# Performance work log

Measured on AMD Instinct MI355X. Metric: run time of the kernel, lower is better.

## Reference

```python
import jax, jax.numpy as jnp
import numpy as np

B, S, E, HEADS, LATENT = 8, 4096, 2048, 16, 64
HEAD_SIZE = E // HEADS  # 128
NEG = -1e20


def setup_inputs() -> dict:
    key = jax.random.key(0)
    k0, k1, k2, k3, k4 = jax.random.split(key, 5)
    return {
        "x": jax.random.normal(k0, (B, S, E), dtype=jnp.float32) * 0.02,
        "W_dkv": jax.random.normal(k1, (LATENT, E), dtype=jnp.float32) * 0.02,
        "W_k": jax.random.normal(k2, (HEAD_SIZE, LATENT), dtype=jnp.float32) * 0.02,
        "W_v": jax.random.normal(k3, (HEAD_SIZE, LATENT), dtype=jnp.float32) * 0.02,
        "W_q": jax.random.normal(k4, (HEAD_SIZE, E), dtype=jnp.float32) * 0.02,
    }


def reference(x, W_dkv, W_k, W_v, W_q):
    # x: [B,S,E]; nn.Linear computes x @ W.T (weight layout [out,in])
    head_size = W_k.shape[0]
    latent = jnp.einsum("bse,le->bsl", x, W_dkv)        # latent KV cache [B,S,L]
    absorbed_q = W_q.T @ W_k                              # [E,H] @ [H,L] -> [E,L]
    q_res = jnp.einsum("bse,el->bsl", x, absorbed_q)     # [B,S,L]
    scale = head_size ** -0.5
    scores = jnp.einsum("bql,bkl->bqk", q_res, latent) * scale  # [B,S,S]
    seq = x.shape[1]
    causal = jnp.tril(jnp.ones((seq, seq), dtype=bool))
    scores = jnp.where(causal, scores, NEG)
    attn = jax.nn.softmax(scores, axis=-1)               # dropout skipped (eval mode)
    v = jnp.einsum("bsl,hl->bsh", latent, W_v)           # compressed V [B,S,H]
    out = jnp.einsum("bqk,bkh->bqh", attn, v)            # [B,S,head_size]
    return out, latent  # latent == kv_cache returned by the module
```

## Files before the change

### kernel.cpp

```cpp
#include <hip/hip_runtime.h>
#include <hip/hip_bf16.h>

#define NB 8
#define NS 4096
#define NE 2048
#define NL 64
#define NH 128
#define NM (NB*NS)
#define NQT (NS/64)

typedef unsigned short ushort_t;
typedef __attribute__((ext_vector_type(4))) float f32x4;
typedef __attribute__((ext_vector_type(8))) __bf16 bf16x8;
typedef __attribute__((ext_vector_type(8))) unsigned short u16x8;
typedef __attribute__((ext_vector_type(4))) unsigned short u16x4;

#define SCALE2 0.1275174537f

__device__ __forceinline__ float fast_exp2(float x) {
    return __builtin_amdgcn_exp2f(x);
}

__device__ __forceinline__ unsigned short f2bf(float f) {
    union { float f; unsigned u; } v; v.f = f;
    unsigned u = v.u + 0x7fffu + ((v.u >> 16) & 1u);
    return (unsigned short)(u >> 16);
}

__device__ __forceinline__ int swz(int row, int colbyte) {
    return (row * 128 + colbyte) ^ ((row & 7) << 4);
}

__device__ __forceinline__ void wg_barrier() {
    asm volatile("s_waitcnt lgkmcnt(0)" ::: "memory");
    __builtin_amdgcn_s_barrier();
    __builtin_amdgcn_sched_barrier(0);
}

__global__ __launch_bounds__(256) void prep_kernel(
    const float* __restrict__ Wdkv, const float* __restrict__ Wk,
    const float* __restrict__ Wq, ushort_t* __restrict__ WcatT)
{
    __shared__ float wk[128 * 64];
    const int t = threadIdx.x;
    for (int i = t; i < 128 * 64; i += 256) wk[i] = Wk[i];
    __syncthreads();
    const int e = blockIdx.x * 256 + t;
    const int l0 = blockIdx.y * 16;
    float acc[16];
    #pragma unroll
    for (int l = 0; l < 16; ++l) acc[l] = 0.f;
    for (int h = 0; h < 128; ++h) {
        float q = Wq[h * NE + e];
        #pragma unroll
        for (int l = 0; l < 16; ++l) acc[l] += q * wk[h * 64 + l0 + l];
    }
    for (int l = 0; l < 16; ++l) WcatT[(64 + l0 + l) * NE + e] = f2bf(acc[l] * SCALE2);
    for (int l = 0; l < 16; ++l) WcatT[(l0 + l) * NE + e] = f2bf(Wdkv[(l0 + l) * NE + e]);
}

__global__ __launch_bounds__(256) void proj_kernel(
    const float* __restrict__ x, const ushort_t* __restrict__ WcatT,
    const float* __restrict__ Wv,
    float* __restrict__ latent_out, ushort_t* __restrict__ k_bf,
    ushort_t* __restrict__ q_bf, ushort_t* __restrict__ v_t)
{
    __shared__ ushort_t As[2][64 * 64];
    __shared__ ushort_t Bs[2][128 * 64];
    const int tid = threadIdx.x;
    const int w = tid >> 6, lane = tid & 63, lg = lane >> 4, li = lane & 15;
    const int m0 = blockIdx.x * 64;
    const int wm = (w >> 1) * 32, wn = (w & 1) * 64;
    const int srow = tid >> 3, scol = tid & 7;

    f32x4 acc[2][4];
    #pragma unroll
    for (int i = 0; i < 2; ++i)
        #pragma unroll
        for (int j = 0; j < 4; ++j) acc[i][j] = f32x4{0.f, 0.f, 0.f, 0.f};

    f32x4 a0reg[2][2], a1reg[2][2];
    u16x8 b0reg[4], b1reg[4];

#define PLOAD(k0, AR, BR) do { \
    _Pragma("unroll") for (int p = 0; p < 2; ++p) { \
        const float* gp = x + (long)(m0 + srow + 32 * p) * NE + (k0) + scol * 8; \
        AR[p][0] = *reinterpret_cast<const f32x4*>(gp); \
        AR[p][1] = *reinterpret_cast<const f32x4*>(gp + 4); } \
    _Pragma("unroll") for (int p = 0; p < 4; ++p) \
        BR[p] = *reinterpret_cast<const u16x8*>(WcatT + (long)(srow + 32 * p) * NE + (k0) + scol * 8); \
} while (0)

#define PWRITE(AR, BR, buf) do { \
    _Pragma("unroll") for (int p = 0; p < 2; ++p) { \
        u16x8 h; \
        _Pragma("unroll") for (int j = 0; j < 4; ++j) { h[j] = f2bf(AR[p][0][j]); h[4 + j] = f2bf(AR[p][1][j]); } \
        *reinterpret_cast<u16x8*>(reinterpret_cast<char*>(As[buf]) + swz(srow + 32 * p, scol * 16)) = h; } \
    _Pragma("unroll") for (int p = 0; p < 4; ++p) \
        *reinterpret_cast<u16x8*>(reinterpret_cast<char*>(Bs[buf]) + swz(srow + 32 * p, scol * 16)) = BR[p]; \
} while (0)

    auto compute = [&](int buf) {
        #pragma unroll
        for (int c = 0; c < 2; ++c) {
            bf16x8 af[2], bfv[4];
            #pragma unroll
            for (int mf = 0; mf < 2; ++mf)
                af[mf] = *reinterpret_cast<const bf16x8*>(
                    reinterpret_cast<const char*>(As[buf]) + swz(wm + 16 * mf + li, c * 64 + lg * 16));
            #pragma unroll
            for (int nf = 0; nf < 4; ++nf)
                bfv[nf] = *reinterpret_cast<const bf16x8*>(
                    reinterpret_cast<const char*>(Bs[buf]) + swz(wn + 16 * nf + li, c * 64 + lg * 16));
            #pragma unroll
            for (int mf = 0; mf < 2; ++mf)
                #pragma unroll
                for (int nf = 0; nf < 4; ++nf)
                    acc[mf][nf] = __builtin_amdgcn_mfma_f32_16x16x32_bf16(
                        af[mf], bfv[nf], acc[mf][nf], 0, 0, 0);
        }
    };

    PLOAD(0, a0reg, b0reg);
    PLOAD(64, a1reg, b1reg);
    PWRITE(a0reg, b0reg, 0);
    wg_barrier();

    for (int ks = 0; ks < 32; ks += 2) {
        if (ks + 2 < 32) PLOAD((ks + 2) * 64, a0reg, b0reg);
        compute(0);
        PWRITE(a1reg, b1reg, 1);
        wg_barrier();
        if (ks + 3 < 32) PLOAD((ks + 3) * 64, a1reg, b1reg);
        compute(1);
        if (ks + 2 < 32) PWRITE(a0reg, b0reg, 0);
        wg_barrier();
    }

    const int b = m0 >> 12, s0 = m0 & 4095;
    #pragma unroll
    for (int mf = 0; mf < 2; ++mf) {
        #pragma unroll
        for (int nf = 0; nf < 4; ++nf) {
            int col = wn + 16 * nf + li;
            #pragma unroll
            for (int r = 0; r < 4; ++r) {
                int row = m0 + wm + 16 * mf + 4 * lg + r;
                float v = acc[mf][nf][r];
                if (wn == 0) {
                    latent_out[(long)row * NL + col] = v;
                    k_bf[(long)row * NL + col] = f2bf(v);
                    *reinterpret_cast<ushort_t*>(reinterpret_cast<char*>(As[0]) +
                        swz(wm + 16 * mf + 4 * lg + r, col * 2)) = f2bf(v);
                } else {
                    q_bf[(long)row * NL + (col - 64)] = f2bf(v);
                }
            }
        }
    }
    {
        const int r = tid >> 1, hf = tid & 1;
        const float* wp = Wv + r * 64 + hf * 32;
        #pragma unroll
        for (int q = 0; q < 2; ++q) {
            f32x4 w0 = *reinterpret_cast<const f32x4*>(wp + q * 16);
            f32x4 w1 = *reinterpret_cast<const f32x4*>(wp + q * 16 + 4);
            f32x4 w2 = *reinterpret_cast<const f32x4*>(wp + q * 16 + 8);
            f32x4 w3 = *reinterpret_cast<const f32x4*>(wp + q * 16 + 12);
            u16x8 h0, h1;
            #pragma unroll
            for (int j = 0; j < 4; ++j) {
                h0[j] = f2bf(w0[j]); h0[4 + j] = f2bf(w1[j]);
                h1[j] = f2bf(w2[j]); h1[4 + j] = f2bf(w3[j]);
            }
            *reinterpret_cast<u16x8*>(reinterpret_cast<char*>(Bs[0]) + swz(r, hf * 64 + q * 32)) = h0;
            *reinterpret_cast<u16x8*>(reinterpret_cast<char*>(Bs[0]) + swz(r, hf * 64 + q * 32 + 16)) = h1;
        }
    }
    wg_barrier();
    f32x4 vacc[2][4];
    #pragma unroll
    for (int i = 0; i < 2; ++i)
        #pragma unroll
        for (int j = 0; j < 4; ++j) vacc[i][j] = f32x4{0.f, 0.f, 0.f, 0.f};
    #pragma unroll
    for (int c = 0; c < 2; ++c) {
        bf16x8 af[2], bfv[4];
        #pragma unroll
        for (int mf = 0; mf < 2; ++mf)
            af[mf] = *reinterpret_cast<const bf16x8*>(
                reinterpret_cast<const char*>(Bs[0]) + swz(32 * w + 16 * mf + li, c * 64 + lg * 16));
        #pragma unroll
        for (int nf = 0; nf < 4; ++nf)
            bfv[nf] = *reinterpret_cast<const bf16x8*>(
                reinterpret_cast<const char*>(As[0]) + swz(16 * nf + li, c * 64 + lg * 16));
        #pragma unroll
        for (int mf = 0; mf < 2; ++mf)
            #pragma unroll
            for (int nf = 0; nf < 4; ++nf)
                vacc[mf][nf] = __builtin_amdgcn_mfma_f32_16x16x32_bf16(
                    af[mf], bfv[nf], vacc[mf][nf], 0, 0, 0);
    }
    #pragma unroll
    for (int mf = 0; mf < 2; ++mf)
        #pragma unroll
        for (int nf = 0; nf < 4; ++nf)
            #pragma unroll
            for (int r = 0; r < 4; ++r)
                v_t[(long)(b * 128 + 32 * w + 16 * mf + 4 * lg + r) * NS + s0 + 16 * nf + li] =
                    f2bf(vacc[mf][nf][r]);
}

__global__ __launch_bounds__(256) void attn_kernel(
    const ushort_t* __restrict__ q_bf, const ushort_t* __restrict__ k_bf,
    const ushort_t* __restrict__ v_t, float* __restrict__ Opart,
    float* __restrict__ lpart, float* __restrict__ mpart)
{
    __shared__ ushort_t Ks[2][64 * 64];
    __shared__ ushort_t Vts[2][128 * 64];
    const int tid = threadIdx.x;
    const int w = tid >> 6, lane = tid & 63, lg = lane >> 4, li = lane & 15;
    const int l = blockIdx.x;
    const int b = l & 7;
    const int j = l >> 3;
    const int h = j >> 6;
    const int p_ = j & 63;
    const int k_ = p_ >> 1, e_ = p_ & 1, kk = (k_ & 15) * 2;
    const int qt = (k_ >> 4) ? (e_ ? kk + 1 : 63 - kk) : (e_ ? 62 - kk : kk);
    const int niter = (qt + 2 - h) >> 1;
    const bool hasdiag = ((qt - h) & 1) == 0;
    const int Q0 = qt << 6;
    const int srow = tid >> 3, scol = tid & 7;
    const int vc0 = 64 * ((scol >> 1) & 1) + 32 * (scol & 1) + 8 * (scol >> 2);

    const long qrow = (long)b * NS + Q0 + 16 * w + li;
    bf16x8 qf[2];
    qf[0] = *reinterpret_cast<const bf16x8*>(q_bf + qrow * NL + 0 + lg * 8);
    qf[1] = *reinterpret_cast<const bf16x8*>(q_bf + qrow * NL + 32 + lg * 8);

    float m_r = -3.0e38f, l_r = 0.f;
    f32x4 oacc[8];
    #pragma unroll
    for (int n = 0; n < 8; ++n) oacc[n] = f32x4{0.f, 0.f, 0.f, 0.f};

    u16x8 k0reg[2], v0reg[4], k1reg[2], v1reg[4];

#define ALOAD(kv0, KR, VR) do { \
    _Pragma("unroll") for (int p = 0; p < 2; ++p) \
        KR[p] = *reinterpret_cast<const u16x8*>(k_bf + ((long)b * NS + (kv0) + srow + 32 * p) * NL + scol * 8); \
    _Pragma("unroll") for (int p = 0; p < 4; ++p) \
        VR[p] = *reinterpret_cast<const u16x8*>(v_t + (long)(b * 128 + srow + 32 * p) * NS + (kv0) + scol * 8); \
} while (0)

#define AWRITE(KR, VR, buf) do { \
    _Pragma("unroll") for (int p = 0; p < 2; ++p) \
        *reinterpret_cast<u16x8*>(reinterpret_cast<char*>(Ks[buf]) + swz(srow + 32 * p, scol * 16)) = KR[p]; \
    _Pragma("unroll") for (int p = 0; p < 4; ++p) { \
        u16x4 lo = {VR[p][0], VR[p][1], VR[p][2], VR[p][3]}; \
        u16x4 hi = {VR[p][4], VR[p][5], VR[p][6], VR[p][7]}; \
        *reinterpret_cast<u16x4*>(reinterpret_cast<char*>(Vts[buf]) + swz(srow + 32 * p, vc0)) = lo; \
        *reinterpret_cast<u16x4*>(reinterpret_cast<char*>(Vts[buf]) + swz(srow + 32 * p, vc0 + 16)) = hi; \
    } \
} while (0)

    auto compute = [&](int buf, bool diag) {
        const char* Kb = reinterpret_cast<const char*>(Ks[buf]);
        const char* Vb = reinterpret_cast<const char*>(Vts[buf]);
        f32x4 s[4];
        #pragma unroll
        for (int f = 0; f < 4; ++f) s[f] = f32x4{0.f, 0.f, 0.f, 0.f};
        __builtin_amdgcn_s_setprio(1);
        #pragma unroll
        for (int c = 0; c < 2; ++c)
            #pragma unroll
            for (int f = 0; f < 4; ++f) {
                bf16x8 a = *reinterpret_cast<const bf16x8*>(Kb + swz(16 * f + li, c * 64 + lg * 16));
                s[f] = __builtin_amdgcn_mfma_f32_16x16x32_bf16(a, qf[c], s[f], 0, 0, 0);
            }
        __builtin_amdgcn_s_setprio(0);
        float p[16];
        float mx = -3.0e38f;
        #pragma unroll
        for (int f = 0; f < 4; ++f)
            #pragma unroll
            for (int r = 0; r < 4; ++r) {
                float v = s[f][r];
                if (diag && (16 * f + 4 * lg + r) > (16 * w + li)) v = -3.0e38f;
                p[f * 4 + r] = v;
                mx = fmaxf(mx, v);
            }
        if (!__all(mx <= m_r + 8.f)) {
            float mxf = fmaxf(mx, __shfl_xor(mx, 16));
            mxf = fmaxf(mxf, __shfl_xor(mxf, 32));
            float m_new = fmaxf(m_r, mxf);
            float corr = fast_exp2(m_r - m_new);
            m_r = m_new;
            l_r *= corr;
            float corrO[4];
            #pragma unroll
            for (int r = 0; r < 4; ++r)
                corrO[r] = __shfl(corr, (lane & 48) | (4 * lg + r));
            #pragma unroll
            for (int n = 0; n < 8; ++n)
                #pragma unroll
                for (int r = 0; r < 4; ++r) oacc[n][r] *= corrO[r];
        }
        float rs = 0.f;
        #pragma unroll
        for (int i = 0; i < 16; ++i) { p[i] = fast_exp2(p[i] - m_r); rs += p[i]; }
        l_r += rs;
        unsigned pw[8];
        #pragma unroll
        for (int f = 0; f < 4; ++f)
            #pragma unroll
            for (int hh = 0; hh < 2; ++hh)
                asm("v_cvt_pk_bf16_f32 %0, %1, %2"
                    : "=v"(pw[2 * f + hh]) : "v"(p[4 * f + 2 * hh]), "v"(p[4 * f + 2 * hh + 1]));
        union { unsigned u[4]; bf16x8 v; } pa0, pa1;
        pa0.u[0] = pw[0]; pa0.u[1] = pw[1]; pa0.u[2] = pw[4]; pa0.u[3] = pw[5];
        pa1.u[0] = pw[2]; pa1.u[1] = pw[3]; pa1.u[2] = pw[6]; pa1.u[3] = pw[7];
        __builtin_amdgcn_s_setprio(1);
        #pragma unroll
        for (int c = 0; c < 2; ++c) {
            bf16x8 pa = c ? pa1.v : pa0.v;
            #pragma unroll
            for (int n = 0; n < 8; ++n) {
                bf16x8 vb = *reinterpret_cast<const bf16x8*>(Vb + swz(16 * n + li, c * 64 + lg * 16));
                oacc[n] = __builtin_amdgcn_mfma_f32_16x16x32_bf16(pa, vb, oacc[n], 0, 0, 0);
            }
        }
        __builtin_amdgcn_s_setprio(0);
    };

    if (niter > 0) {
        ALOAD(h * 64, k0reg, v0reg);
        if (niter >= 2) ALOAD((h + 2) * 64, k1reg, v1reg);
        AWRITE(k0reg, v0reg, 0);
        wg_barrier();
        for (int i = 0; i < niter; i += 2) {
            if (i + 2 < niter) ALOAD((h + 2 * (i + 2)) * 64, k0reg, v0reg);
            compute(0, hasdiag && (i == niter - 1));
            if (i + 1 < niter) AWRITE(k1reg, v1reg, 1);
            wg_barrier();
            if (i + 1 >= niter) break;
            if (i + 3 < niter) ALOAD((h + 2 * (i + 3)) * 64, k1reg, v1reg);
            compute(1, hasdiag && (i + 1 == niter - 1));
            if (i + 2 < niter) AWRITE(k0reg, v0reg, 0);
            wg_barrier();
        }
    }

    l_r += __shfl_xor(l_r, 16);
    l_r += __shfl_xor(l_r, 32);
    const int IB = ((h * NB + b) << 6) + qt;
    if (lane < 16)  {
        lpart[IB * 64 + 16 * w + li] = l_r;
        mpart[IB * 64 + 16 * w + li] = m_r;
    }
    #pragma unroll
    for (int n = 0; n < 8; ++n)
        #pragma unroll
        for (int r = 0; r < 4; ++r)
            Opart[((long)IB * 64 + 16 * w + 4 * lg + r) * NH + 16 * n + li] = oacc[n][r];
}

__global__ __launch_bounds__(256) void merge_kernel(
    const float* __restrict__ Opart, const float* __restrict__ lpart,
    const float* __restrict__ mpart, float* __restrict__ out)
{
    const int blk = blockIdx.x;
    const int b = blk >> 6, qt = blk & 63;
    const int t = threadIdx.x;
    const int row = t >> 2, c0 = (t & 3) * 4;
    const int IB1 = (b << 6) + qt;
    const int IB2 = ((NB + b) << 6) + qt;
    const long r1 = (long)IB1 * 64 + row, r2 = (long)IB2 * 64 + row;
    float l1 = lpart[r1], m1 = mpart[r1];
    float l2 = lpart[r2], m2 = mpart[r2];
    float M = fmaxf(m1, m2);
    float w1 = fast_exp2(m1 - M), w2 = fast_exp2(m2 - M);
    float inv = 1.f / (w1 * l1 + w2 * l2);
    float a1 = w1 * inv, a2 = w2 * inv;
    const float* o1 = Opart + r1 * NH;
    const float* o2 = Opart + r2 * NH;
    float* op = out + ((long)b * NS + qt * 64 + row) * NH;
    #pragma unroll
    for (int jj = 0; jj < 8; ++jj) {
        int col = c0 + 16 * jj;
        f32x4 A = *reinterpret_cast<const f32x4*>(o1 + col);
        f32x4 Bv = *reinterpret_cast<const f32x4*>(o2 + col);
        f32x4 R;
        #pragma unroll
        for (int q = 0; q < 4; ++q) R[q] = A[q] * a1 + Bv[q] * a2;
        *reinterpret_cast<f32x4*>(op + col) = R;
    }
}

extern "C" void kernel_launch(void* const* d_in, const int* in_sizes, int n_in,
                              void* d_out, int out_size, void* d_ws, size_t ws_size,
                              hipStream_t stream) {
    const float* x    = (const float*)d_in[0];
    const float* Wdkv = (const float*)d_in[1];
    const float* Wk   = (const float*)d_in[2];
    const float* Wv   = (const float*)d_in[3];
    const float* Wq   = (const float*)d_in[4];

    float* out = (float*)d_out;
    float* latent_out = out + (long)NM * NH;

    ushort_t* WcatT = (ushort_t*)d_ws;
    ushort_t* q_bf  = WcatT + 128 * NE;
    ushort_t* k_bf  = q_bf + (long)NM * NL;
    ushort_t* v_t   = k_bf + (long)NM * NL;
    float* Opart = (float*)(v_t + (long)NM * NH);
    float* lpart = Opart + (long)2 * NB * NQT * 64 * NH;
    float* mpart = lpart + 2 * NB * NQT * 64;

    hipLaunchKernelGGL(prep_kernel, dim3(NE / 256, 4), dim3(256), 0, stream, Wdkv, Wk, Wq, WcatT);
    hipLaunchKernelGGL(proj_kernel, dim3(NM / 64), dim3(256), 0, stream,
                       x, WcatT, Wv, latent_out, k_bf, q_bf, v_t);
    hipLaunchKernelGGL(attn_kernel, dim3(1024), dim3(256), 0, stream,
                       q_bf, k_bf, v_t, Opart, lpart, mpart);
    hipLaunchKernelGGL(merge_kernel, dim3(NB * NQT), dim3(256), 0, stream,
                       Opart, lpart, mpart, out);
}
```

Measured before the change: 161.1 us.

## Attend over latent values and apply W_v after the softmax merge

Uses associativity (attn @ (latent @ Wv^T) = (attn @ latent) @ Wv^T): the attention kernel now accumulates P·latent in the 64-wide latent space instead of the 128-wide V space. The projection kernel writes a transposed latent (made with an identity-matrix MFMA) rather than computing V, and the merge kernel applies W_v once per query tile with MFMAs. This halves the V tile loads, LDS traffic, PV MFMAs and the partial-output size. In exchange the merge kernel does more work, including an extra bf16 rounding of the merged output before the W_v product.

```diff
diff --git a/kernel.cpp b/kernel.cpp
--- a/kernel.cpp
+++ b/kernel.cpp
@@ -61,9 +61,8 @@
 
 __global__ __launch_bounds__(256) void proj_kernel(
     const float* __restrict__ x, const ushort_t* __restrict__ WcatT,
-    const float* __restrict__ Wv,
     float* __restrict__ latent_out, ushort_t* __restrict__ k_bf,
-    ushort_t* __restrict__ q_bf, ushort_t* __restrict__ v_t)
+    ushort_t* __restrict__ q_bf, ushort_t* __restrict__ kt)
 {
     __shared__ ushort_t As[2][64 * 64];
     __shared__ ushort_t Bs[2][128 * 64];
@@ -158,66 +157,36 @@
             }
         }
     }
-    {
-        const int r = tid >> 1, hf = tid & 1;
-        const float* wp = Wv + r * 64 + hf * 32;
-        #pragma unroll
-        for (int q = 0; q < 2; ++q) {
-            f32x4 w0 = *reinterpret_cast<const f32x4*>(wp + q * 16);
-            f32x4 w1 = *reinterpret_cast<const f32x4*>(wp + q * 16 + 4);
-            f32x4 w2 = *reinterpret_cast<const f32x4*>(wp + q * 16 + 8);
-            f32x4 w3 = *reinterpret_cast<const f32x4*>(wp + q * 16 + 12);
-            u16x8 h0, h1;
-            #pragma unroll
-            for (int j = 0; j < 4; ++j) {
-                h0[j] = f2bf(w0[j]); h0[4 + j] = f2bf(w1[j]);
-                h1[j] = f2bf(w2[j]); h1[4 + j] = f2bf(w3[j]);
-            }
-            *reinterpret_cast<u16x8*>(reinterpret_cast<char*>(Bs[0]) + swz(r, hf * 64 + q * 32)) = h0;
-            *reinterpret_cast<u16x8*>(reinterpret_cast<char*>(Bs[0]) + swz(r, hf * 64 + q * 32 + 16)) = h1;
-        }
-    }
     wg_barrier();
-    f32x4 vacc[2][4];
-    #pragma unroll
-    for (int i = 0; i < 2; ++i)
-        #pragma unroll
-        for (int j = 0; j < 4; ++j) vacc[i][j] = f32x4{0.f, 0.f, 0.f, 0.f};
-    #pragma unroll
-    for (int c = 0; c < 2; ++c) {
-        bf16x8 af[2], bfv[4];
-        #pragma unroll
-        for (int mf = 0; mf < 2; ++mf)
-            af[mf] = *reinterpret_cast<const bf16x8*>(
-                reinterpret_cast<const char*>(Bs[0]) + swz(32 * w + 16 * mf + li, c * 64 + lg * 16));
-        #pragma unroll
-        for (int nf = 0; nf < 4; ++nf)
-            bfv[nf] = *reinterpret_cast<const bf16x8*>(
-                reinterpret_cast<const char*>(As[0]) + swz(16 * nf + li, c * 64 + lg * 16));
-        #pragma unroll
-        for (int mf = 0; mf < 2; ++mf)
-            #pragma unroll
-            for (int nf = 0; nf < 4; ++nf)
-                vacc[mf][nf] = __builtin_amdgcn_mfma_f32_16x16x32_bf16(
-                    af[mf], bfv[nf], vacc[mf][nf], 0, 0, 0);
-    }
-    #pragma unroll
-    for (int mf = 0; mf < 2; ++mf)
-        #pragma unroll
-        for (int nf = 0; nf < 4; ++nf)
-            #pragma unroll
-            for (int r = 0; r < 4; ++r)
-                v_t[(long)(b * 128 + 32 * w + 16 * mf + 4 * lg + r) * NS + s0 + 16 * nf + li] =
-                    f2bf(vacc[mf][nf][r]);
+    union { u16x8 u; bf16x8 v; } iu;
+    #pragma unroll
+    for (int j = 0; j < 8; ++j)
+        iu.u[j] = (lg == (li >> 3) + 2 * (w & 1) && (li & 7) == j)
+                      ? (ushort_t)0x3F80 : (ushort_t)0;
+    const int ckt = w >> 1;
+    f32x4 ktacc[4];
+    #pragma unroll
+    for (int nf = 0; nf < 4; ++nf) {
+        bf16x8 bfv = *reinterpret_cast<const bf16x8*>(
+            reinterpret_cast<const char*>(As[0]) + swz(16 * nf + li, ckt * 64 + lg * 16));
+        ktacc[nf] = __builtin_amdgcn_mfma_f32_16x16x32_bf16(
+            iu.v, bfv, f32x4{0.f, 0.f, 0.f, 0.f}, 0, 0, 0);
+    }
+    #pragma unroll
+    for (int nf = 0; nf < 4; ++nf)
+        #pragma unroll
+        for (int r = 0; r < 4; ++r)
+            kt[(long)(b * 64 + 16 * w + 4 * lg + r) * NS + s0 + 16 * nf + li] =
+                f2bf(ktacc[nf][r]);
 }
 
 __global__ __launch_bounds__(256) void attn_kernel(
     const ushort_t* __restrict__ q_bf, const ushort_t* __restrict__ k_bf,
-    const ushort_t* __restrict__ v_t, float* __restrict__ Opart,
+    const ushort_t* __restrict__ kt, float* __restrict__ Opart,
     float* __restrict__ lpart, float* __restrict__ mpart)
 {
     __shared__ ushort_t Ks[2][64 * 64];
-    __shared__ ushort_t Vts[2][128 * 64];
+    __shared__ ushort_t KTs[2][64 * 64];
     const int tid = threadIdx.x;
     const int w = tid >> 6, lane = tid & 63, lg = lane >> 4, li = lane & 15;
     const int l = blockIdx.x;
@@ -239,33 +208,33 @@
     qf[1] = *reinterpret_cast<const bf16x8*>(q_bf + qrow * NL + 32 + lg * 8);
 
     float m_r = -3.0e38f, l_r = 0.f;
-    f32x4 oacc[8];
-    #pragma unroll
-    for (int n = 0; n < 8; ++n) oacc[n] = f32x4{0.f, 0.f, 0.f, 0.f};
-
-    u16x8 k0reg[2], v0reg[4], k1reg[2], v1reg[4];
-
-#define ALOAD(kv0, KR, VR) do { \
+    f32x4 oacc[4];
+    #pragma unroll
+    for (int n = 0; n < 4; ++n) oacc[n] = f32x4{0.f, 0.f, 0.f, 0.f};
+
+    u16x8 k0reg[2], t0reg[2], k1reg[2], t1reg[2];
+
+#define ALOAD(kv0, KR, TR) do { \
     _Pragma("unroll") for (int p = 0; p < 2; ++p) \
         KR[p] = *reinterpret_cast<const u16x8*>(k_bf + ((long)b * NS + (kv0) + srow + 32 * p) * NL + scol * 8); \
-    _Pragma("unroll") for (int p = 0; p < 4; ++p) \
-        VR[p] = *reinterpret_cast<const u16x8*>(v_t + (long)(b * 128 + srow + 32 * p) * NS + (kv0) + scol * 8); \
+    _Pragma("unroll") for (int p = 0; p < 2; ++p) \
+        TR[p] = *reinterpret_cast<const u16x8*>(kt + (long)(b * 64 + srow + 32 * p) * NS + (kv0) + scol * 8); \
 } while (0)
 
-#define AWRITE(KR, VR, buf) do { \
+#define AWRITE(KR, TR, buf) do { \
     _Pragma("unroll") for (int p = 0; p < 2; ++p) \
         *reinterpret_cast<u16x8*>(reinterpret_cast<char*>(Ks[buf]) + swz(srow + 32 * p, scol * 16)) = KR[p]; \
-    _Pragma("unroll") for (int p = 0; p < 4; ++p) { \
-        u16x4 lo = {VR[p][0], VR[p][1], VR[p][2], VR[p][3]}; \
-        u16x4 hi = {VR[p][4], VR[p][5], VR[p][6], VR[p][7]}; \
-        *reinterpret_cast<u16x4*>(reinterpret_cast<char*>(Vts[buf]) + swz(srow + 32 * p, vc0)) = lo; \
-        *reinterpret_cast<u16x4*>(reinterpret_cast<char*>(Vts[buf]) + swz(srow + 32 * p, vc0 + 16)) = hi; \
+    _Pragma("unroll") for (int p = 0; p < 2; ++p) { \
+        u16x4 lo = {TR[p][0], TR[p][1], TR[p][2], TR[p][3]}; \
+        u16x4 hi = {TR[p][4], TR[p][5], TR[p][6], TR[p][7]}; \
+        *reinterpret_cast<u16x4*>(reinterpret_cast<char*>(KTs[buf]) + swz(srow + 32 * p, vc0)) = lo; \
+        *reinterpret_cast<u16x4*>(reinterpret_cast<char*>(KTs[buf]) + swz(srow + 32 * p, vc0 + 16)) = hi; \
     } \
 } while (0)
 
     auto compute = [&](int buf, bool diag) {
         const char* Kb = reinterpret_cast<const char*>(Ks[buf]);
-        const char* Vb = reinterpret_cast<const char*>(Vts[buf]);
+        const char* Tb = reinterpret_cast<const char*>(KTs[buf]);
         f32x4 s[4];
         #pragma unroll
         for (int f = 0; f < 4; ++f) s[f] = f32x4{0.f, 0.f, 0.f, 0.f};
@@ -301,7 +270,7 @@
             for (int r = 0; r < 4; ++r)
                 corrO[r] = __shfl(corr, (lane & 48) | (4 * lg + r));
             #pragma unroll
-            for (int n = 0; n < 8; ++n)
+            for (int n = 0; n < 4; ++n)
                 #pragma unroll
                 for (int r = 0; r < 4; ++r) oacc[n][r] *= corrO[r];
         }
@@ -324,8 +293,8 @@
         for (int c = 0; c < 2; ++c) {
             bf16x8 pa = c ? pa1.v : pa0.v;
             #pragma unroll
-            for (int n = 0; n < 8; ++n) {
-                bf16x8 vb = *reinterpret_cast<const bf16x8*>(Vb + swz(16 * n + li, c * 64 + lg * 16));
+            for (int n = 0; n < 4; ++n) {
+                bf16x8 vb = *reinterpret_cast<const bf16x8*>(Tb + swz(16 * n + li, c * 64 + lg * 16));
                 oacc[n] = __builtin_amdgcn_mfma_f32_16x16x32_bf16(pa, vb, oacc[n], 0, 0, 0);
             }
         }
@@ -333,19 +302,19 @@
     };
 
     if (niter > 0) {
-        ALOAD(h * 64, k0reg, v0reg);
-        if (niter >= 2) ALOAD((h + 2) * 64, k1reg, v1reg);
-        AWRITE(k0reg, v0reg, 0);
+        ALOAD(h * 64, k0reg, t0reg);
+        if (niter >= 2) ALOAD((h + 2) * 64, k1reg, t1reg);
+        AWRITE(k0reg, t0reg, 0);
         wg_barrier();
         for (int i = 0; i < niter; i += 2) {
-            if (i + 2 < niter) ALOAD((h + 2 * (i + 2)) * 64, k0reg, v0reg);
+            if (i + 2 < niter) ALOAD((h + 2 * (i + 2)) * 64, k0reg, t0reg);
             compute(0, hasdiag && (i == niter - 1));
-            if (i + 1 < niter) AWRITE(k1reg, v1reg, 1);
+            if (i + 1 < niter) AWRITE(k1reg, t1reg, 1);
             wg_barrier();
             if (i + 1 >= niter) break;
-            if (i + 3 < niter) ALOAD((h + 2 * (i + 3)) * 64, k1reg, v1reg);
+            if (i + 3 < niter) ALOAD((h + 2 * (i + 3)) * 64, k1reg, t1reg);
             compute(1, hasdiag && (i + 1 == niter - 1));
-            if (i + 2 < niter) AWRITE(k0reg, v0reg, 0);
+            if (i + 2 < niter) AWRITE(k0reg, t0reg, 0);
             wg_barrier();
         }
     }
@@ -358,41 +327,106 @@
         mpart[IB * 64 + 16 * w + li] = m_r;
     }
     #pragma unroll
-    for (int n = 0; n < 8; ++n)
+    for (int n = 0; n < 4; ++n)
         #pragma unroll
         for (int r = 0; r < 4; ++r)
-            Opart[((long)IB * 64 + 16 * w + 4 * lg + r) * NH + 16 * n + li] = oacc[n][r];
+            Opart[((long)IB * 64 + 16 * w + 4 * lg + r) * NL + 16 * n + li] = oacc[n][r];
 }
 
 __global__ __launch_bounds__(256) void merge_kernel(
     const float* __restrict__ Opart, const float* __restrict__ lpart,
-    const float* __restrict__ mpart, float* __restrict__ out)
+    const float* __restrict__ mpart, const float* __restrict__ Wv,
+    float* __restrict__ out)
 {
+    __shared__ ushort_t Ms[64 * 64];
+    __shared__ ushort_t Wvs[128 * 64];
+    __shared__ float Os[64 * 132];
     const int blk = blockIdx.x;
     const int b = blk >> 6, qt = blk & 63;
-    const int t = threadIdx.x;
-    const int row = t >> 2, c0 = (t & 3) * 4;
-    const int IB1 = (b << 6) + qt;
-    const int IB2 = ((NB + b) << 6) + qt;
-    const long r1 = (long)IB1 * 64 + row, r2 = (long)IB2 * 64 + row;
-    float l1 = lpart[r1], m1 = mpart[r1];
-    float l2 = lpart[r2], m2 = mpart[r2];
-    float M = fmaxf(m1, m2);
-    float w1 = fast_exp2(m1 - M), w2 = fast_exp2(m2 - M);
-    float inv = 1.f / (w1 * l1 + w2 * l2);
-    float a1 = w1 * inv, a2 = w2 * inv;
-    const float* o1 = Opart + r1 * NH;
-    const float* o2 = Opart + r2 * NH;
-    float* op = out + ((long)b * NS + qt * 64 + row) * NH;
-    #pragma unroll
-    for (int jj = 0; jj < 8; ++jj) {
-        int col = c0 + 16 * jj;
-        f32x4 A = *reinterpret_cast<const f32x4*>(o1 + col);
-        f32x4 Bv = *reinterpret_cast<const f32x4*>(o2 + col);
-        f32x4 R;
-        #pragma unroll
-        for (int q = 0; q < 4; ++q) R[q] = A[q] * a1 + Bv[q] * a2;
-        *reinterpret_cast<f32x4*>(op + col) = R;
+    const int tid = threadIdx.x;
+    const int w = tid >> 6, lane = tid & 63, lg = lane >> 4, li = lane & 15;
+
+    {
+        const int r = tid >> 1, hf = tid & 1;
+        const float* wp = Wv + r * 64 + hf * 32;
+        #pragma unroll
+        for (int q = 0; q < 2; ++q) {
+            f32x4 w0 = *reinterpret_cast<const f32x4*>(wp + q * 16);
+            f32x4 w1 = *reinterpret_cast<const f32x4*>(wp + q * 16 + 4);
+            f32x4 w2 = *reinterpret_cast<const f32x4*>(wp + q * 16 + 8);
+            f32x4 w3 = *reinterpret_cast<const f32x4*>(wp + q * 16 + 12);
+            u16x8 h0, h1;
+            #pragma unroll
+            for (int jj = 0; jj < 4; ++jj) {
+                h0[jj] = f2bf(w0[jj]); h0[4 + jj] = f2bf(w1[jj]);
+                h1[jj] = f2bf(w2[jj]); h1[4 + jj] = f2bf(w3[jj]);
+            }
+            *reinterpret_cast<u16x8*>(reinterpret_cast<char*>(Wvs) + swz(r, hf * 64 + q * 32)) = h0;
+            *reinterpret_cast<u16x8*>(reinterpret_cast<char*>(Wvs) + swz(r, hf * 64 + q * 32 + 16)) = h1;
+        }
+    }
+    {
+        const int r = tid >> 2, c0 = (tid & 3) * 16;
+        const long L1 = ((long)((b << 6) + qt)) * 64 + r;
+        const long L2 = ((long)(((NB + b) << 6) + qt)) * 64 + r;
+        float l1 = lpart[L1], m1 = mpart[L1];
+        float l2 = lpart[L2], m2 = mpart[L2];
+        float M = fmaxf(m1, m2);
+        float w1 = fast_exp2(m1 - M), w2 = fast_exp2(m2 - M);
+        float inv = 1.f / (w1 * l1 + w2 * l2);
+        float a1 = w1 * inv, a2 = w2 * inv;
+        const float* o1 = Opart + L1 * NL;
+        const float* o2 = Opart + L2 * NL;
+        #pragma unroll
+        for (int q = 0; q < 4; ++q) {
+            int col = c0 + q * 4;
+            f32x4 A = *reinterpret_cast<const f32x4*>(o1 + col);
+            f32x4 Bv = *reinterpret_cast<const f32x4*>(o2 + col);
+            u16x4 hh;
+            #pragma unroll
+            for (int k = 0; k < 4; ++k) hh[k] = f2bf(A[k] * a1 + Bv[k] * a2);
+            *reinterpret_cast<u16x4*>(reinterpret_cast<char*>(Ms) + swz(r, col * 2)) = hh;
+        }
+    }
+    __syncthreads();
+    f32x4 vacc[2][4];
+    #pragma unroll
+    for (int i = 0; i < 2; ++i)
+        #pragma unroll
+        for (int jj = 0; jj < 4; ++jj) vacc[i][jj] = f32x4{0.f, 0.f, 0.f, 0.f};
+    #pragma unroll
+    for (int c = 0; c < 2; ++c) {
+        bf16x8 af[2], bfv[4];
+        #pragma unroll
+        for (int mf = 0; mf < 2; ++mf)
+            af[mf] = *reinterpret_cast<const bf16x8*>(
+                reinterpret_cast<const char*>(Wvs) + swz(32 * w + 16 * mf + li, c * 64 + lg * 16));
+        #pragma unroll
+        for (int nf = 0; nf < 4; ++nf)
+            bfv[nf] = *reinterpret_cast<const bf16x8*>(
+                reinterpret_cast<const char*>(Ms) + swz(16 * nf + li, c * 64 + lg * 16));
+        #pragma unroll
+        for (int mf = 0; mf < 2; ++mf)
+            #pragma unroll
+            for (int nf = 0; nf < 4; ++nf)
+                vacc[mf][nf] = __builtin_amdgcn_mfma_f32_16x16x32_bf16(
+                    af[mf], bfv[nf], vacc[mf][nf], 0, 0, 0);
+    }
+    #pragma unroll
+    for (int mf = 0; mf < 2; ++mf)
+        #pragma unroll
+        for (int nf = 0; nf < 4; ++nf)
+            #pragma unroll
+            for (int r = 0; r < 4; ++r)
+                Os[(16 * nf + li) * 132 + 32 * w + 16 * mf + 4 * lg + r] = vacc[mf][nf][r];
+    __syncthreads();
+    {
+        const int r = tid >> 2, cb = (tid & 3) * 32;
+        float* op = out + ((long)b * NS + qt * 64 + r) * NH + cb;
+        const float* sp = Os + r * 132 + cb;
+        #pragma unroll
+        for (int q = 0; q < 8; ++q)
+            *reinterpret_cast<f32x4*>(op + 4 * q) = *reinterpret_cast<const f32x4*>(sp + 4 * q);
     }
 }
 
@@ -411,16 +445,16 @@
     ushort_t* WcatT = (ushort_t*)d_ws;
     ushort_t* q_bf  = WcatT + 128 * NE;
     ushort_t* k_bf  = q_bf + (long)NM * NL;
-    ushort_t* v_t   = k_bf + (long)NM * NL;
-    float* Opart = (float*)(v_t + (long)NM * NH);
-    float* lpart = Opart + (long)2 * NB * NQT * 64 * NH;
+    ushort_t* kt    = k_bf + (long)NM * NL;
+    float* Opart = (float*)(kt + (long)NM * NL);
+    float* lpart = Opart + (long)2 * NB * NQT * 64 * NL;
     float* mpart = lpart + 2 * NB * NQT * 64;
 
     hipLaunchKernelGGL(prep_kernel, dim3(NE / 256, 4), dim3(256), 0, stream, Wdkv, Wk, Wq, WcatT);
     hipLaunchKernelGGL(proj_kernel, dim3(NM / 64), dim3(256), 0, stream,
-                       x, WcatT, Wv, latent_out, k_bf, q_bf, v_t);
+                       x, WcatT, latent_out, k_bf, q_bf, kt);
     hipLaunchKernelGGL(attn_kernel, dim3(1024), dim3(256), 0, stream,
-                       q_bf, k_bf, v_t, Opart, lpart, mpart);
+                       q_bf, k_bf, kt, Opart, lpart, mpart);
     hipLaunchKernelGGL(merge_kernel, dim3(NB * NQT), dim3(256), 0, stream,
-                       Opart, lpart, mpart, out);
-}
+                       Opart, lpart, mpart, Wv, out);
+}
```

Result: faster. 142.8 us (-11.3%).
